# Optimization experiments

Measured on AMD Instinct MI355X. Metric: run time of the kernel, lower is better.

Reference implementation:

```python
import jax, jax.numpy as jnp
import numpy as np

B, S, D = 16, 4096, 64
SCALE = float(np.sqrt(D))  # sqrt(hidden_size)


def setup_inputs() -> dict:
    key = jax.random.key(0)
    kq, kk, kv = jax.random.split(key, 3)
    return {
        "query": jax.random.normal(kq, (B, S, D), dtype=jnp.float32),
        "key": jax.random.normal(kk, (B, S, D), dtype=jnp.float32),
        "value": jax.random.normal(kv, (B, S, D), dtype=jnp.float32),
    }


def reference(query, key, value):
    # energy: [B, S, S]
    energy = jnp.einsum("bqd,bkd->bqk", query, key) / SCALE
    attention = jax.nn.softmax(energy, axis=2)
    return jnp.einsum("bqk,bkd->bqd", attention, value)
```

## Files before the change

kernel.cpp:

```cpp
#include <hip/hip_runtime.h>


#define NBATCH 16
#define SEQ    4096
#define DIM    64
#define BQ     256
#define BK     64
#define NKT    (SEQ / BK)
#define KHALF  (NKT / 2)
#define OELEMS (NBATCH * SEQ * DIM)
#define NROWS  (NBATCH * SEQ)

#define QSCALE 0.180336879f

typedef _Float16 half2_t __attribute__((ext_vector_type(2)));
typedef _Float16 half4_t __attribute__((ext_vector_type(4)));
typedef _Float16 half8_t __attribute__((ext_vector_type(8)));
typedef float    floatx4 __attribute__((ext_vector_type(4)));

__device__ inline float fast_exp2(float x) {
#if __has_builtin(__builtin_amdgcn_exp2f)
  return __builtin_amdgcn_exp2f(x);
#else
  return exp2f(x);
#endif
}
__device__ inline float fast_rcp(float x) {
#if __has_builtin(__builtin_amdgcn_rcpf)
  return __builtin_amdgcn_rcpf(x);
#else
  return 1.0f / x;
#endif
}

__device__ inline int swz(int row, int col) {
  return row * 64 + ((((col >> 3) ^ ((row >> 1) & 7)) << 3) | (col & 7));
}

__global__ __launch_bounds__(256, 2)
void attn_f16_flash(const float* __restrict__ Qg, const float* __restrict__ Kg,
                    const float* __restrict__ Vg, float* __restrict__ O0g,
                    float* __restrict__ O1g, float* __restrict__ lsg)
{
  __shared__ __align__(16) _Float16 sK[64 * 64];
  __shared__ __align__(16) _Float16 sV[64 * 64];

  const int tid  = threadIdx.x;
  const int wave = tid >> 6;
  const int lane = tid & 63;
  const int l16  = lane & 15;
  const int quad = lane >> 4;
  const int hK   = (l16 >> 1) & 7;

  const int t16 = tid & 15;
  const int kg  = tid >> 4;

  const int bid  = blockIdx.x;
  const int half = bid & 1;
  const int qb   = bid >> 1;
  const int b    = qb >> 4;
  const int qt   = qb & 15;
  const int q0   = qt * BQ + wave * 64;
  const int kt0  = half * KHALF;

  const float* Qb = Qg + ((size_t)b * SEQ + q0) * DIM;
  const float* Kb = Kg + (size_t)b * SEQ * DIM;
  const float* Vb = Vg + (size_t)b * SEQ * DIM;
  float*       Ob = (half ? O1g : O0g) + ((size_t)b * SEQ + q0) * DIM;
  float*       Ls = lsg + half * NROWS + b * SEQ + q0;

  half8_t qf[4][2];
  #pragma unroll
  for (int s = 0; s < 4; ++s)
    #pragma unroll
    for (int c = 0; c < 2; ++c) {
      const floatx4 f0 = *(const floatx4*)(Qb + (s * 16 + l16) * DIM + c * 32 + quad * 8);
      const floatx4 f1 = *(const floatx4*)(Qb + (s * 16 + l16) * DIM + c * 32 + quad * 8 + 4);
      half8_t h;
      #pragma unroll
      for (int j = 0; j < 4; ++j) h[j] = (_Float16)(f0[j] * QSCALE);
      #pragma unroll
      for (int j = 0; j < 4; ++j) h[4 + j] = (_Float16)(f1[j] * QSCALE);
      qf[s][c] = h;
    }

  floatx4 oacc2[4][4];
  float   lsum2[4];
  #pragma unroll
  for (int n = 0; n < 4; ++n)
    #pragma unroll
    for (int s = 0; s < 4; ++s) oacc2[n][s] = (floatx4){0.f, 0.f, 0.f, 0.f};
  #pragma unroll
  for (int s = 0; s < 4; ++s) lsum2[s] = 0.f;

  floatx4 kbuf[4], vbuf[4];

  #define LOAD_TILE(KT)                                                        \
    do {                                                                       \
      const float* Kt_ = Kb + (size_t)(KT) * BK * DIM;                         \
      const float* Vt_ = Vb + (size_t)(KT) * BK * DIM;                         \
      _Pragma("unroll")                                                        \
      for (int i = 0; i < 4; ++i) {                                            \
        const int key = kg + 16 * i;                                           \
        kbuf[i] = *(const floatx4*)(Kt_ + key * DIM + t16 * 4);                \
        vbuf[i] = *(const floatx4*)(Vt_ + key * DIM + t16 * 4);                \
      }                                                                        \
    } while (0)

  #define WRITE_TILE()                                                         \
    do {                                                                       \
      _Pragma("unroll")                                                        \
      for (int i = 0; i < 4; ++i) {                                            \
        const int key = kg + 16 * i;                                           \
        half4_t h;                                                             \
        _Pragma("unroll")                                                      \
        for (int j = 0; j < 4; ++j) h[j] = (_Float16)kbuf[i][j];               \
        *(half4_t*)&sK[swz(key, t16 * 4)] = h;                                 \
      }                                                                        \
      {                                                                        \
        const int vbase = (kg >> 2) * 8 + (kg & 3) * 2;                        \
        _Pragma("unroll")                                                      \
        for (int e = 0; e < 4; ++e) {                                          \
          const int dim = t16 * 4 + e;                                         \
          half2_t h0; h0[0] = (_Float16)vbuf[0][e]; h0[1] = (_Float16)vbuf[1][e];\
          half2_t h1; h1[0] = (_Float16)vbuf[2][e]; h1[1] = (_Float16)vbuf[3][e];\
          *(half2_t*)&sV[swz(dim, vbase)]      = h0;                           \
          *(half2_t*)&sV[swz(dim, vbase + 32)] = h1;                           \
        }                                                                      \
      }                                                                        \
    } while (0)

  #define COMPUTE_TILE()                                                       \
    do {                                                                       \
      floatx4 sc[4][4];                           \
      _Pragma("unroll")                                                        \
      for (int nk = 0; nk < 4; ++nk)                                           \
        _Pragma("unroll")                                                      \
        for (int s = 0; s < 4; ++s) sc[nk][s] = (floatx4){0.f, 0.f, 0.f, 0.f}; \
                         \
      _Pragma("unroll")                                                        \
      for (int nk = 0; nk < 4; ++nk)                                           \
        _Pragma("unroll")                                                      \
        for (int c = 0; c < 2; ++c) {                                          \
          half8_t kf = *(const half8_t*)&sK[(nk * 16 + l16) * 64 +             \
                                            (((c * 4 + quad) ^ hK) << 3)];     \
          _Pragma("unroll")                                                    \
          for (int s = 0; s < 4; ++s)                                          \
            sc[nk][s] = __builtin_amdgcn_mfma_f32_16x16x32_f16(kf, qf[s][c],   \
                                                               sc[nk][s], 0, 0, 0);\
        }                                                                      \
              \
      half8_t bfrag[4][2];                                                     \
      _Pragma("unroll")                                                        \
      for (int s = 0; s < 4; ++s)                                              \
        _Pragma("unroll")                                                      \
        for (int c = 0; c < 2; ++c) {                                          \
          half8_t bf;                                                          \
          _Pragma("unroll")                                                    \
          for (int j = 0; j < 8; ++j) {                                        \
            float p = fast_exp2(sc[(c << 1) | (j & 1)][s][j >> 1]);            \
            lsum2[s] += p;                                                     \
            bf[j] = (_Float16)p;                                               \
          }                                                                    \
          bfrag[s][c] = bf;                                                    \
        }                                                                      \
                  \
      _Pragma("unroll")                                                        \
      for (int c = 0; c < 2; ++c)                                              \
        _Pragma("unroll")                                                      \
        for (int n = 0; n < 4; ++n) {                                          \
          half8_t vf = *(const half8_t*)&sV[(n * 16 + l16) * 64 +              \
                                            (((c * 4 + quad) ^ hK) << 3)];     \
          _Pragma("unroll")                                                    \
          for (int s = 0; s < 4; ++s)                                          \
            oacc2[n][s] = __builtin_amdgcn_mfma_f32_16x16x32_f16(vf, bfrag[s][c],\
                                                                 oacc2[n][s], 0, 0, 0);\
        }                                                                      \
    } while (0)

  LOAD_TILE(kt0);
  WRITE_TILE();
  __syncthreads();

  #pragma unroll 1
  for (int kt = kt0; kt < kt0 + KHALF - 1; ++kt) {
    LOAD_TILE(kt + 1);
    COMPUTE_TILE();
    __syncthreads();
    WRITE_TILE();
    __syncthreads();
  }
  COMPUTE_TILE();

  #pragma unroll
  for (int s = 0; s < 4; ++s) {
    float v = lsum2[s];
    v += __shfl_xor(v, 16);
    v += __shfl_xor(v, 32);
    if (lane < 16) Ls[s * 16 + l16] = v;
  }
  #pragma unroll
  for (int s = 0; s < 4; ++s)
    #pragma unroll
    for (int n = 0; n < 4; ++n)
      *(floatx4*)&Ob[(s * 16 + l16) * DIM + n * 16 + quad * 4] = oacc2[n][s];

  #undef LOAD_TILE
  #undef WRITE_TILE
  #undef COMPUTE_TILE
}

__global__ __launch_bounds__(256)
void attn_combine(float* __restrict__ O, const float* __restrict__ O1,
                  const float* __restrict__ lsg)
{
  const int i = blockIdx.x * 256 + threadIdx.x;
  const float* l0 = lsg;
  const float* l1 = lsg + NROWS;
  const int row = i >> 4;
  const float inv = fast_rcp(l0[row] + l1[row]);
  const float4 a  = ((const float4*)O)[i];
  const float4 bb = ((const float4*)O1)[i];
  float4 r;
  r.x = (a.x + bb.x) * inv;
  r.y = (a.y + bb.y) * inv;
  r.z = (a.z + bb.z) * inv;
  r.w = (a.w + bb.w) * inv;
  ((float4*)O)[i] = r;
}

extern "C" void kernel_launch(void* const* d_in, const int* in_sizes, int n_in,
                              void* d_out, int out_size, void* d_ws, size_t ws_size,
                              hipStream_t stream) {
  const float* Q = (const float*)d_in[0];
  const float* K = (const float*)d_in[1];
  const float* V = (const float*)d_in[2];
  float* O  = (float*)d_out;
  float* O1 = (float*)d_ws;
  float* Ls = (float*)d_ws + OELEMS;
  (void)in_sizes; (void)n_in; (void)out_size; (void)ws_size;

  attn_f16_flash<<<dim3(2 * NBATCH * (SEQ / BQ)), dim3(256), 0, stream>>>(Q, K, V, O, O1, Ls);
  attn_combine<<<dim3(OELEMS / 4 / 256), dim3(256), 0, stream>>>(O, O1, Ls);
}
```

Measured before the change: 168.4 us.

## Prepack K/V to fp16 swizzled tiles and stream via async global-to-LDS double buffering

Adds a prepack kernel that converts K and V to fp16 once, in the swizzled (and transposed for V) LDS tile layout, and writes them to workspace. The attention kernel then copies those tiles straight into double-buffered shared memory with global_load_lds, which removes the per-block fp32 loads, conversions and LDS scatter stores on every tile. The QK/softmax/PV step is split into two 32-key halves to lower peak register use. In exchange it adds an extra kernel launch, a global round trip for the fp16 copies, and twice the LDS per block, which may limit occupancy.

```diff
diff --git a/kernel.cpp b/kernel.cpp
--- a/kernel.cpp
+++ b/kernel.cpp
@@ -10,6 +10,8 @@
 #define KHALF  (NKT / 2)
 #define OELEMS (NBATCH * SEQ * DIM)
 #define NROWS  (NBATCH * SEQ)
+#define NTILES (NBATCH * NKT)
+#define TILEH  4096
 
 #define QSCALE 0.180336879f
 
@@ -37,13 +39,66 @@
   return row * 64 + ((((col >> 3) ^ ((row >> 1) & 7)) << 3) | (col & 7));
 }
 
+__device__ inline void async16(const void* g, void* l) {
+  __builtin_amdgcn_global_load_lds(
+      (const __attribute__((address_space(1))) void*)g,
+      (__attribute__((address_space(3))) void*)l, 16, 0, 0);
+}
+
 __global__ __launch_bounds__(256, 2)
-void attn_f16_flash(const float* __restrict__ Qg, const float* __restrict__ Kg,
-                    const float* __restrict__ Vg, float* __restrict__ O0g,
+void prepack_kv(const float* __restrict__ Kg, const float* __restrict__ Vg,
+                _Float16* __restrict__ Kh, _Float16* __restrict__ Vh)
+{
+  __shared__ __align__(16) _Float16 sKi[TILEH];
+  __shared__ __align__(16) _Float16 sVi[TILEH];
+  const int tid = threadIdx.x;
+  const int t16 = tid & 15;
+  const int kg  = tid >> 4;
+  const int bt  = blockIdx.x;
+  const float* Kt_ = Kg + (size_t)bt * BK * DIM;
+  const float* Vt_ = Vg + (size_t)bt * BK * DIM;
+
+  floatx4 kbuf[4], vbuf[4];
+  #pragma unroll
+  for (int i = 0; i < 4; ++i) {
+    const int key = kg + 16 * i;
+    kbuf[i] = *(const floatx4*)(Kt_ + key * DIM + t16 * 4);
+    vbuf[i] = *(const floatx4*)(Vt_ + key * DIM + t16 * 4);
+  }
+  #pragma unroll
+  for (int i = 0; i < 4; ++i) {
+    const int key = kg + 16 * i;
+    half4_t h;
+    #pragma unroll
+    for (int j = 0; j < 4; ++j) h[j] = (_Float16)kbuf[i][j];
+    *(half4_t*)&sKi[swz(key, t16 * 4)] = h;
+  }
+  {
+    const int vbase = (kg >> 2) * 8 + (kg & 3) * 2;
+    #pragma unroll
+    for (int e = 0; e < 4; ++e) {
+      const int dim = t16 * 4 + e;
+      half2_t h0; h0[0] = (_Float16)vbuf[0][e]; h0[1] = (_Float16)vbuf[1][e];
+      half2_t h1; h1[0] = (_Float16)vbuf[2][e]; h1[1] = (_Float16)vbuf[3][e];
+      *(half2_t*)&sVi[swz(dim, vbase)]      = h0;
+      *(half2_t*)&sVi[swz(dim, vbase + 32)] = h1;
+    }
+  }
+  __syncthreads();
+  half8_t* Ko = (half8_t*)(Kh + (size_t)bt * TILEH);
+  half8_t* Vo = (half8_t*)(Vh + (size_t)bt * TILEH);
+  const half8_t* Ks = (const half8_t*)sKi;
+  const half8_t* Vs = (const half8_t*)sVi;
+  Ko[tid] = Ks[tid]; Ko[tid + 256] = Ks[tid + 256];
+  Vo[tid] = Vs[tid]; Vo[tid + 256] = Vs[tid + 256];
+}
+
+__global__ __launch_bounds__(256, 2)
+void attn_f16_flash(const float* __restrict__ Qg, const _Float16* __restrict__ Kh,
+                    const _Float16* __restrict__ Vh, float* __restrict__ O0g,
                     float* __restrict__ O1g, float* __restrict__ lsg)
 {
-  __shared__ __align__(16) _Float16 sK[64 * 64];
-  __shared__ __align__(16) _Float16 sV[64 * 64];
+  __shared__ __align__(16) _Float16 sT[2][2 * TILEH];
 
   const int tid  = threadIdx.x;
   const int wave = tid >> 6;
@@ -51,9 +106,6 @@
   const int l16  = lane & 15;
   const int quad = lane >> 4;
   const int hK   = (l16 >> 1) & 7;
-
-  const int t16 = tid & 15;
-  const int kg  = tid >> 4;
 
   const int bid  = blockIdx.x;
   const int half = bid & 1;
@@ -64,10 +116,8 @@
   const int kt0  = half * KHALF;
 
   const float* Qb = Qg + ((size_t)b * SEQ + q0) * DIM;
-  const float* Kb = Kg + (size_t)b * SEQ * DIM;
-  const float* Vb = Vg + (size_t)b * SEQ * DIM;
   float*       Ob = (half ? O1g : O0g) + ((size_t)b * SEQ + q0) * DIM;
-  float*       Ls = lsg + half * NROWS + b * SEQ + q0;
+  float*       Ls = lsg + (size_t)half * NROWS + b * SEQ + q0;
 
   half8_t qf[4][2];
   #pragma unroll
@@ -93,104 +143,84 @@
   #pragma unroll
   for (int s = 0; s < 4; ++s) lsum2[s] = 0.f;
 
-  floatx4 kbuf[4], vbuf[4];
-
-  #define LOAD_TILE(KT)                                                        \
+  #define ASYNC(KT, BUF)                                                       \
     do {                                                                       \
-      const float* Kt_ = Kb + (size_t)(KT) * BK * DIM;                         \
-      const float* Vt_ = Vb + (size_t)(KT) * BK * DIM;                         \
+      const char* gk = (const char*)(Kh + ((size_t)b * NKT + (KT)) * TILEH)    \
+                       + wave * 2048;                                          \
+      const char* gv = (const char*)(Vh + ((size_t)b * NKT + (KT)) * TILEH)    \
+                       + wave * 2048;                                          \
+      char* lk = (char*)(&sT[BUF][0])     + wave * 2048;                       \
+      char* lv = (char*)(&sT[BUF][TILEH]) + wave * 2048;                       \
+      async16(gk + lane * 16,        lk);                                      \
+      async16(gk + 1024 + lane * 16, lk + 1024);                               \
+      async16(gv + lane * 16,        lv);                                      \
+      async16(gv + 1024 + lane * 16, lv + 1024);                               \
+    } while (0)
+
+  #define COMPUTE(BUF)                                                         \
+    do {                                                                       \
+      const _Float16* SKB = &sT[BUF][0];                                       \
+      const _Float16* SVB = &sT[BUF][TILEH];                                   \
       _Pragma("unroll")                                                        \
-      for (int i = 0; i < 4; ++i) {                                            \
-        const int key = kg + 16 * i;                                           \
-        kbuf[i] = *(const floatx4*)(Kt_ + key * DIM + t16 * 4);                \
-        vbuf[i] = *(const floatx4*)(Vt_ + key * DIM + t16 * 4);                \
-      }                                                                        \
-    } while (0)
-
-  #define WRITE_TILE()                                                         \
-    do {                                                                       \
-      _Pragma("unroll")                                                        \
-      for (int i = 0; i < 4; ++i) {                                            \
-        const int key = kg + 16 * i;                                           \
-        half4_t h;                                                             \
-        _Pragma("unroll")                                                      \
-        for (int j = 0; j < 4; ++j) h[j] = (_Float16)kbuf[i][j];               \
-        *(half4_t*)&sK[swz(key, t16 * 4)] = h;                                 \
-      }                                                                        \
-      {                                                                        \
-        const int vbase = (kg >> 2) * 8 + (kg & 3) * 2;                        \
-        _Pragma("unroll")                                                      \
-        for (int e = 0; e < 4; ++e) {                                          \
-          const int dim = t16 * 4 + e;                                         \
-          half2_t h0; h0[0] = (_Float16)vbuf[0][e]; h0[1] = (_Float16)vbuf[1][e];\
-          half2_t h1; h1[0] = (_Float16)vbuf[2][e]; h1[1] = (_Float16)vbuf[3][e];\
-          *(half2_t*)&sV[swz(dim, vbase)]      = h0;                           \
-          *(half2_t*)&sV[swz(dim, vbase + 32)] = h1;                           \
+      for (int h = 0; h < 2; ++h) {                                            \
+        floatx4 sc2[2][4];                                                     \
+        _Pragma("unroll")                                                      \
+        for (int k2 = 0; k2 < 2; ++k2)                                         \
+          _Pragma("unroll")                                                    \
+          for (int s = 0; s < 4; ++s) sc2[k2][s] = (floatx4){0.f, 0.f, 0.f, 0.f};\
+        _Pragma("unroll")                                                      \
+        for (int k2 = 0; k2 < 2; ++k2) {                                       \
+          const int nk = h * 2 + k2;                                           \
+          _Pragma("unroll")                                                    \
+          for (int c = 0; c < 2; ++c) {                                        \
+            half8_t kf = *(const half8_t*)&SKB[(nk * 16 + l16) * 64 +          \
+                                               (((c * 4 + quad) ^ hK) << 3)];  \
+            _Pragma("unroll")                                                  \
+            for (int s = 0; s < 4; ++s)                                        \
+              sc2[k2][s] = __builtin_amdgcn_mfma_f32_16x16x32_f16(             \
+                  kf, qf[s][c], sc2[k2][s], 0, 0, 0);                          \
+          }                                                                    \
+        }                                                                      \
+        half8_t bfr[4];                                                        \
+        _Pragma("unroll")                                                      \
+        for (int s = 0; s < 4; ++s) {                                          \
+          half8_t bf;                                                          \
+          _Pragma("unroll")                                                    \
+          for (int j = 0; j < 8; ++j) {                                        \
+            float p = fast_exp2(sc2[j & 1][s][j >> 1]);                        \
+            lsum2[s] += p;                                                     \
+            bf[j] = (_Float16)p;                                               \
+          }                                                                    \
+          bfr[s] = bf;                                                         \
+        }                                                                      \
+        _Pragma("unroll")                                                      \
+        for (int n = 0; n < 4; ++n) {                                          \
+          half8_t vf = *(const half8_t*)&SVB[(n * 16 + l16) * 64 +             \
+                                             (((h * 4 + quad) ^ hK) << 3)];    \
+          _Pragma("unroll")                                                    \
+          for (int s = 0; s < 4; ++s)                                          \
+            oacc2[n][s] = __builtin_amdgcn_mfma_f32_16x16x32_f16(              \
+                vf, bfr[s], oacc2[n][s], 0, 0, 0);                             \
         }                                                                      \
       }                                                                        \
     } while (0)
 
-  #define COMPUTE_TILE()                                                       \
-    do {                                                                       \
-      floatx4 sc[4][4];                           \
-      _Pragma("unroll")                                                        \
-      for (int nk = 0; nk < 4; ++nk)                                           \
-        _Pragma("unroll")                                                      \
-        for (int s = 0; s < 4; ++s) sc[nk][s] = (floatx4){0.f, 0.f, 0.f, 0.f}; \
-                         \
-      _Pragma("unroll")                                                        \
-      for (int nk = 0; nk < 4; ++nk)                                           \
-        _Pragma("unroll")                                                      \
-        for (int c = 0; c < 2; ++c) {                                          \
-          half8_t kf = *(const half8_t*)&sK[(nk * 16 + l16) * 64 +             \
-                                            (((c * 4 + quad) ^ hK) << 3)];     \
-          _Pragma("unroll")                                                    \
-          for (int s = 0; s < 4; ++s)                                          \
-            sc[nk][s] = __builtin_amdgcn_mfma_f32_16x16x32_f16(kf, qf[s][c],   \
-                                                               sc[nk][s], 0, 0, 0);\
-        }                                                                      \
-              \
-      half8_t bfrag[4][2];                                                     \
-      _Pragma("unroll")                                                        \
-      for (int s = 0; s < 4; ++s)                                              \
-        _Pragma("unroll")                                                      \
-        for (int c = 0; c < 2; ++c) {                                          \
-          half8_t bf;                                                          \
-          _Pragma("unroll")                                                    \
-          for (int j = 0; j < 8; ++j) {                                        \
-            float p = fast_exp2(sc[(c << 1) | (j & 1)][s][j >> 1]);            \
-            lsum2[s] += p;                                                     \
-            bf[j] = (_Float16)p;                                               \
-          }                                                                    \
-          bfrag[s][c] = bf;                                                    \
-        }                                                                      \
-                  \
-      _Pragma("unroll")                                                        \
-      for (int c = 0; c < 2; ++c)                                              \
-        _Pragma("unroll")                                                      \
-        for (int n = 0; n < 4; ++n) {                                          \
-          half8_t vf = *(const half8_t*)&sV[(n * 16 + l16) * 64 +              \
-                                            (((c * 4 + quad) ^ hK) << 3)];     \
-          _Pragma("unroll")                                                    \
-          for (int s = 0; s < 4; ++s)                                          \
-            oacc2[n][s] = __builtin_amdgcn_mfma_f32_16x16x32_f16(vf, bfrag[s][c],\
-                                                                 oacc2[n][s], 0, 0, 0);\
-        }                                                                      \
-    } while (0)
-
-  LOAD_TILE(kt0);
-  WRITE_TILE();
+  ASYNC(kt0, 0);
   __syncthreads();
 
   #pragma unroll 1
-  for (int kt = kt0; kt < kt0 + KHALF - 1; ++kt) {
-    LOAD_TILE(kt + 1);
-    COMPUTE_TILE();
+  for (int t = 0; t < (KHALF - 2) / 2; ++t) {
+    ASYNC(kt0 + 2 * t + 1, 1);
+    COMPUTE(0);
     __syncthreads();
-    WRITE_TILE();
+    ASYNC(kt0 + 2 * t + 2, 0);
+    COMPUTE(1);
     __syncthreads();
   }
-  COMPUTE_TILE();
+  ASYNC(kt0 + KHALF - 1, 1);
+  COMPUTE(0);
+  __syncthreads();
+  COMPUTE(1);
 
   #pragma unroll
   for (int s = 0; s < 4; ++s) {
@@ -205,9 +235,8 @@
     for (int n = 0; n < 4; ++n)
       *(floatx4*)&Ob[(s * 16 + l16) * DIM + n * 16 + quad * 4] = oacc2[n][s];
 
-  #undef LOAD_TILE
-  #undef WRITE_TILE
-  #undef COMPUTE_TILE
+  #undef ASYNC
+  #undef COMPUTE
 }
 
 __global__ __launch_bounds__(256)
@@ -215,10 +244,8 @@
                   const float* __restrict__ lsg)
 {
   const int i = blockIdx.x * 256 + threadIdx.x;
-  const float* l0 = lsg;
-  const float* l1 = lsg + NROWS;
   const int row = i >> 4;
-  const float inv = fast_rcp(l0[row] + l1[row]);
+  const float inv = fast_rcp(lsg[row] + lsg[NROWS + row]);
   const float4 a  = ((const float4*)O)[i];
   const float4 bb = ((const float4*)O1)[i];
   float4 r;
@@ -236,10 +263,15 @@
   const float* K = (const float*)d_in[1];
   const float* V = (const float*)d_in[2];
   float* O  = (float*)d_out;
-  float* O1 = (float*)d_ws;
-  float* Ls = (float*)d_ws + OELEMS;
   (void)in_sizes; (void)n_in; (void)out_size; (void)ws_size;
 
-  attn_f16_flash<<<dim3(2 * NBATCH * (SEQ / BQ)), dim3(256), 0, stream>>>(Q, K, V, O, O1, Ls);
+  float*     O1 = (float*)d_ws;
+  float*     Ls = O1 + OELEMS;
+  _Float16*  Kh = (_Float16*)(Ls + 2 * NROWS);
+  _Float16*  Vh = Kh + (size_t)NTILES * TILEH;
+
+  prepack_kv<<<dim3(NTILES), dim3(256), 0, stream>>>(K, V, Kh, Vh);
+  attn_f16_flash<<<dim3(2 * NBATCH * (SEQ / BQ)), dim3(256), 0, stream>>>(
+      Q, Kh, Vh, O, O1, Ls);
   attn_combine<<<dim3(OELEMS / 4 / 256), dim3(256), 0, stream>>>(O, O1, Ls);
 }
```

Result: no change. 166.9 us (-0.9%).
